# Performance work log

Hardware: AMD Instinct MI355X
Metric: run time of the kernel (lower is better)

Reference implementation:

```python
import jax, jax.numpy as jnp
import numpy as np

B, T, H, P, N = 32, 512, 128, 16, 16
D = 4 * H


def _lstm(x, Wih, Whh, bih, bhh):
    # standard torch-style LSTM, batch_first input x: [B, T, 1], zero init state
    Bz = x.shape[0]
    Hh = Whh.shape[1]
    h0 = jnp.zeros((Bz, Hh), x.dtype)

    def step(carry, xt):
        h, c = carry
        g = xt @ Wih.T + bih + h @ Whh.T + bhh  # [B, 4H], gate order i,f,g,o
        i, f, gg, o = jnp.split(g, 4, axis=-1)
        c = jax.nn.sigmoid(f) * c + jax.nn.sigmoid(i) * jnp.tanh(gg)
        h = jax.nn.sigmoid(o) * jnp.tanh(c)
        return (h, c), h

    _, hs = jax.lax.scan(step, (h0, h0), jnp.swapaxes(x, 0, 1))
    return jnp.swapaxes(hs, 0, 1)  # [B, T, H]


def _forward(Y, Xp, Xn, Xi, init_c, init_h, Wih, Whh, bih, bhh,
             Wc, Uc, bc, Wg, Ug, bg, Wf, Uf, bf, Wo, Uo, bo, Wa,
             Watt, batt, vatt, W1, b1, W2, b2, W3, b3):
    run = lambda x: _lstm(x, Wih, Whh, bih, bhh)
    Y1 = run(Y)                                              # [B,T,H]
    Xi1 = run(Xi)
    Xp1 = jnp.mean(jax.vmap(run)(jnp.moveaxis(Xp, 1, 0)), axis=0)  # mean over P stocks
    Xn1 = jnp.mean(jax.vmap(run)(jnp.moveaxis(Xn, 1, 0)), axis=0)
    result = jnp.concatenate([Y1, Xp1, Xn1, Xi1], axis=2)    # [B,T,4H]

    Hh = Wa.shape[0]

    def mi_step(carry, xt):  # Mi-LSTM cell: 4 input streams with gated-candidate attention
        c, h = carry
        xs = xt.reshape(xt.shape[0], 4, Hh)                  # split 4H into 4 streams
        cand = jnp.tanh(jnp.einsum('bkh,khj->bkj', xs, Wc) + jnp.einsum('bh,khj->bkj', h, Uc) + bc)
        ig = jax.nn.sigmoid(jnp.einsum('bkh,khj->bkj', xs, Wg) + jnp.einsum('bh,khj->bkj', h, Ug) + bg)
        l = ig * cand                                        # [B,4,H]
        a = jax.nn.softmax(jnp.einsum('bkj,bj->bk', l, c @ Wa), axis=1)
        lmix = jnp.einsum('bk,bkj->bj', a, l)
        f = jax.nn.sigmoid(xt @ Wf + h @ Uf + bf)
        o = jax.nn.sigmoid(xt @ Wo + h @ Uo + bo)
        c = f * c + lmix
        h = o * jnp.tanh(c)
        return (c, h), h

    _, hs = jax.lax.scan(mi_step, (init_c, init_h), jnp.swapaxes(result, 0, 1))
    Y2 = jnp.swapaxes(hs, 0, 1)                              # [B,T,H]

    # temporal attention over the Mi-LSTM outputs
    scores = jnp.tanh(Y2 @ Watt + batt) @ vatt               # [B,T]
    attw = jax.nn.softmax(scores, axis=1)
    Y3 = jnp.einsum('bt,bth->bh', attw, Y2)                  # [B,H]

    hm = jax.nn.relu(Y3 @ W1 + b1)
    hm = jax.nn.relu(hm @ W2 + b2)
    return hm @ W3 + b3                                      # [B,1]


def setup_inputs() -> dict:
    key = jax.random.key(0)
    ks = jax.random.split(key, 24)
    u = lambda k, s: jax.random.uniform(k, s, dtype=jnp.float32)
    nr = lambda k, s: jax.random.normal(k, s, dtype=jnp.float32) * 0.05
    z = lambda s: jnp.zeros(s, jnp.float32)
    return {
        'Y': u(ks[0], (B, T, 1)), 'Xp': u(ks[1], (B, P, T, 1)), 'Xn': u(ks[2], (B, N, T, 1)),
        'Xi': u(ks[3], (B, T, 1)), 'Target': u(ks[4], (B, 1)),
        'init_c': u(ks[5], (B, H)), 'init_h': u(ks[6], (B, H)),
        'Wih': nr(ks[7], (4 * H, 1)), 'Whh': nr(ks[8], (4 * H, H)), 'bih': z(4 * H), 'bhh': z(4 * H),
        'Wc': nr(ks[9], (4, H, H)), 'Uc': nr(ks[10], (4, H, H)), 'bc': z((4, H)),
        'Wg': nr(ks[11], (4, H, H)), 'Ug': nr(ks[12], (4, H, H)), 'bg': z((4, H)),
        'Wf': nr(ks[13], (D, H)), 'Uf': nr(ks[14], (H, H)), 'bf': z(H),
        'Wo': nr(ks[15], (D, H)), 'Uo': nr(ks[16], (H, H)), 'bo': z(H),
        'Wa': nr(ks[17], (H, H)),
        'Watt': nr(ks[18], (H, H)), 'batt': z(H), 'vatt': nr(ks[19], (H,)),
        'W1': nr(ks[20], (H, H)), 'b1': z(H),
        'W2': nr(ks[21], (H, H)), 'b2': z(H),
        'W3': nr(ks[22], (H, 1)), 'b3': z(1),
    }


def reference(Y, Xp, Xn, Xi, Target, init_c, init_h, Wih, Whh, bih, bhh,
              Wc, Uc, bc, Wg, Ug, bg, Wf, Uf, bf, Wo, Uo, bo, Wa,
              Watt, batt, vatt, W1, b1, W2, b2, W3, b3):
    out = _forward(Y, Xp, Xn, Xi, init_c, init_h, Wih, Whh, bih, bhh,
                   Wc, Uc, bc, Wg, Ug, bg, Wf, Uf, bf, Wo, Uo, bo, Wa,
                   Watt, batt, vatt, W1, b1, W2, b2, W3, b3)
    loss = jnp.mean((out - Target) ** 2)
    return out, loss
```

## Files before the change

kernel.cpp:

```cpp
#include <hip/hip_runtime.h>
#include <hip/hip_fp16.h>

typedef _Float16 half8 __attribute__((ext_vector_type(8)));
typedef float float4_ __attribute__((ext_vector_type(4)));

__device__ __forceinline__ float rcp_(float x) { return __builtin_amdgcn_rcpf(x); }
__device__ __forceinline__ float sigf(float x) { return rcp_(1.f + __expf(-x)); }
__device__ __forceinline__ float tanhf2(float x) {
  x = fminf(fmaxf(x, -15.f), 15.f);
  float e = __expf(-2.f * x);
  return (1.f - e) * rcp_(1.f + e);
}

#define DOT2F16(acc, w, h) asm("v_dot2_f32_f16 %0, %1, %2, %0" : "+v"(acc) : "v"(w), "v"(h))

__global__ __launch_bounds__(512, 2)
void k1_lstm(const float* __restrict__ Y, const float* __restrict__ Xp,
             const float* __restrict__ Xn, const float* __restrict__ Xi,
             const float* __restrict__ Wih, const float* __restrict__ Whh,
             const float* __restrict__ bih, const float* __restrict__ bhh,
             _Float16* __restrict__ result)
{
  __shared__ float x_lds[16][513];
  __shared__ _Float16 hbuf[2][16][136];

  const int tid  = threadIdx.x;
  const int wv   = tid >> 6;
  const int lane = tid & 63;
  const int cl   = lane & 15;
  const int rowg = lane >> 4;
  const int bid  = blockIdx.x;

  const float* xsrc; int slot; int do_mean; int b_out_base;
  if (bid < 2)       { xsrc = Y  + (size_t)(bid * 16) * 512;        slot = 0; do_mean = 0; b_out_base = bid * 16; }
  else if (bid < 4)  { xsrc = Xi + (size_t)((bid - 2) * 16) * 512;  slot = 3; do_mean = 0; b_out_base = (bid - 2) * 16; }
  else if (bid < 36) { xsrc = Xp + (size_t)((bid - 4) * 16) * 512;  slot = 1; do_mean = 1; b_out_base = bid - 4; }
  else               { xsrc = Xn + (size_t)((bid - 36) * 16) * 512; slot = 2; do_mean = 1; b_out_base = bid - 36; }

  for (int i = tid; i < 16 * 512; i += 512) {
    int r = i >> 9, t = i & 511;
    x_lds[r][t] = xsrc[r * 512 + t];
  }
  for (int i = tid; i < 16 * 136; i += 512) {
    hbuf[0][i / 136][i % 136] = (_Float16)0.f;
  }

  const int cg = wv * 16 + cl;
  half8 bw[4][4];
  #pragma unroll
  for (int g = 0; g < 4; ++g) {
    #pragma unroll
    for (int kc = 0; kc < 4; ++kc) {
      const float* p = Whh + (size_t)(g * 128 + cg) * 128 + kc * 32 + rowg * 8;
      half8 v;
      #pragma unroll
      for (int j = 0; j < 8; ++j) v[j] = (_Float16)p[j];
      bw[g][kc] = v;
    }
  }
  float wih_r[4], bias_r[4];
  #pragma unroll
  for (int g = 0; g < 4; ++g) {
    wih_r[g]  = Wih[g * 128 + cg];
    bias_r[g] = bih[g * 128 + cg] + bhh[g * 128 + cg];
  }

  float c_reg[4] = {0.f, 0.f, 0.f, 0.f};
  float hvp[4] = {0.f, 0.f, 0.f, 0.f};
  float sprev = 0.f;
  __syncthreads();

  for (int t = 0; t < 512; ++t) {
    if (t > 0) {
      if (!do_mean) {
        #pragma unroll
        for (int i = 0; i < 4; ++i) {
          int b = b_out_base + rowg * 4 + i;
          result[(((size_t)b * 512 + (t - 1)) * 4 + slot) * 128 + cg] = (_Float16)hvp[i];
        }
      } else {
        if (rowg == 0)
          result[(((size_t)b_out_base * 512 + (t - 1)) * 4 + slot) * 128 + cg] = (_Float16)sprev;
      }
    }

    const int cur = t & 1;
    half8 a[4];
    #pragma unroll
    for (int kc = 0; kc < 4; ++kc)
      a[kc] = *(const half8*)&hbuf[cur][cl][kc * 32 + rowg * 8];

    float4_ acc[4];
    #pragma unroll
    for (int g = 0; g < 4; ++g) {
      float4_ z = {0.f, 0.f, 0.f, 0.f};
      #pragma unroll
      for (int kc = 0; kc < 4; ++kc)
        z = __builtin_amdgcn_mfma_f32_16x16x32_f16(a[kc], bw[g][kc], z, 0, 0, 0);
      acc[g] = z;
    }

    float hv[4];
    #pragma unroll
    for (int i = 0; i < 4; ++i) {
      const int row = rowg * 4 + i;
      float x  = x_lds[row][t];
      float ui = acc[0][i] + x * wih_r[0] + bias_r[0];
      float uf = acc[1][i] + x * wih_r[1] + bias_r[1];
      float ug = acc[2][i] + x * wih_r[2] + bias_r[2];
      float uo = acc[3][i] + x * wih_r[3] + bias_r[3];
      float ii = sigf(ui), ff = sigf(uf), gg = tanhf2(ug), oo = sigf(uo);
      float c  = ff * c_reg[i] + ii * gg;
      c_reg[i] = c;
      float h  = oo * tanhf2(c);
      hv[i] = h;
      hbuf[cur ^ 1][row][cg] = (_Float16)h;
    }

    if (!do_mean) {
      #pragma unroll
      for (int i = 0; i < 4; ++i) hvp[i] = hv[i];
    } else {
      float s = hv[0] + hv[1] + hv[2] + hv[3];
      s += __shfl_xor(s, 16, 64);
      s += __shfl_xor(s, 32, 64);
      sprev = s * 0.0625f;
    }
    __syncthreads();
  }

  if (!do_mean) {
    #pragma unroll
    for (int i = 0; i < 4; ++i) {
      int b = b_out_base + rowg * 4 + i;
      result[(((size_t)b * 512 + 511) * 4 + slot) * 128 + cg] = (_Float16)hvp[i];
    }
  } else {
    if (rowg == 0)
      result[(((size_t)b_out_base * 512 + 511) * 4 + slot) * 128 + cg] = (_Float16)sprev;
  }
}

__global__ __launch_bounds__(512, 2)
void k2_gemm(const _Float16* __restrict__ result,
             const float* __restrict__ Wc, const float* __restrict__ Wg,
             const float* __restrict__ Wf, const float* __restrict__ Wo,
             _Float16* __restrict__ candX, _Float16* __restrict__ igX,
             _Float16* __restrict__ fX, _Float16* __restrict__ oX)
{
  __shared__ _Float16 a_lds[128][136];
  __shared__ _Float16 bt_lds[256][136];

  const int tid   = threadIdx.x;
  const int lane  = tid & 63;
  const int wv    = tid >> 6;
  const int cl    = lane & 15, rowg = lane >> 4;
  const int mtile = blockIdx.x;
  const int role  = blockIdx.y;

  const int nchunks = (role == 0) ? 4 : 1;
  const int kstream = role - 1;

  float4_ acc[16];
  #pragma unroll
  for (int n = 0; n < 16; ++n) acc[n] = (float4_){0.f, 0.f, 0.f, 0.f};

  for (int ch = 0; ch < nchunks; ++ch) {
    const int koff = (role == 0) ? ch * 128 : kstream * 128;
    for (int i = tid; i < 1024; i += 512) {
      int r = i >> 3, v8 = i & 7;
      half8 val = *(const half8*)&result[((size_t)(mtile * 128 + r)) * 512 + koff + v8 * 8];
      *(half8*)&a_lds[r][v8 * 8] = val;
    }
    for (int i = tid; i < 128 * 256; i += 512) {
      int n = i & 255, kk = i >> 8;
      float w;
      if (role == 0) {
        w = (n < 128) ? Wf[(size_t)(ch * 128 + kk) * 128 + n]
                      : Wo[(size_t)(ch * 128 + kk) * 128 + (n - 128)];
      } else {
        w = (n < 128) ? Wc[(size_t)(kstream * 128 + kk) * 128 + n]
                      : Wg[(size_t)(kstream * 128 + kk) * 128 + (n - 128)];
      }
      bt_lds[n][kk] = (_Float16)w;
    }
    __syncthreads();
    #pragma unroll
    for (int kc = 0; kc < 4; ++kc) {
      half8 a = *(const half8*)&a_lds[wv * 16 + cl][kc * 32 + rowg * 8];
      #pragma unroll
      for (int n = 0; n < 16; ++n) {
        half8 bb = *(const half8*)&bt_lds[n * 16 + cl][kc * 32 + rowg * 8];
        acc[n] = __builtin_amdgcn_mfma_f32_16x16x32_f16(a, bb, acc[n], 0, 0, 0);
      }
    }
    __syncthreads();
  }

  #pragma unroll
  for (int n = 0; n < 16; ++n) {
    int col = n * 16 + cl;
    #pragma unroll
    for (int i = 0; i < 4; ++i) {
      size_t r = (size_t)mtile * 128 + wv * 16 + rowg * 4 + i;
      _Float16 v = (_Float16)acc[n][i];
      if (role == 0) {
        if (col < 128) fX[r * 128 + col] = v;
        else           oX[r * 128 + (col - 128)] = v;
      } else {
        if (col < 128) candX[(r * 4 + kstream) * 128 + col] = v;
        else           igX  [(r * 4 + kstream) * 128 + (col - 128)] = v;
      }
    }
  }
}

#define PRELOAD(arr, sbase)                                                 \
  {                                                                         \
    const int s = tid + sbase;                                              \
    const float* src; float mul = 1.f;                                      \
    if (s < 512)       src = Uc + (s >> 7) * 16384 + (s & 127);             \
    else if (s < 1024) src = Ug + ((s >> 7) - 4) * 16384 + (s & 127);       \
    else if (s < 1152) src = Uf + (s - 1024);                               \
    else if (s < 1280) src = Uo + (s - 1152);                               \
    else if (s < 1408) src = Wa + (s - 1280);                               \
    else             { src = Wa; mul = 0.f; }                               \
    _Pragma("unroll")                                                       \
    for (int d = 0; d < 64; ++d) {                                          \
      union { _Float16 h[2]; unsigned u; } cv;                              \
      cv.h[0] = (_Float16)(src[(2 * d) * 128] * mul);                       \
      cv.h[1] = (_Float16)(src[(2 * d + 1) * 128] * mul);                   \
      arr[d] = cv.u;                                                        \
    }                                                                       \
  }

__global__ __launch_bounds__(512, 1)
void k3_scan(const float* __restrict__ Uc, const float* __restrict__ Ug,
             const float* __restrict__ Uf, const float* __restrict__ Uo,
             const float* __restrict__ Wa,
             const float* __restrict__ bc, const float* __restrict__ bg,
             const float* __restrict__ bfv, const float* __restrict__ bov,
             const float* __restrict__ init_c, const float* __restrict__ init_h,
             const _Float16* __restrict__ candX, const _Float16* __restrict__ igX,
             const _Float16* __restrict__ fX, const _Float16* __restrict__ oX,
             _Float16* __restrict__ Y2)
{
  __shared__ __align__(16) unsigned h_pk[64];
  __shared__ __align__(16) unsigned c_pk[64];
  __shared__ float c_f32[128];
  __shared__ float raw[1536];
  __shared__ float part2[2][4];

  const int tid = threadIdx.x;
  const int b   = blockIdx.x;

  unsigned wpk0[64], wpk1[64], wpk2[64];
  PRELOAD(wpk0, 0)
  PRELOAD(wpk1, 512)
  PRELOAD(wpk2, 1024)

  float bc_r[4] = {0, 0, 0, 0}, bg_r[4] = {0, 0, 0, 0}, bf_r = 0.f, bo_r = 0.f;
  if (tid < 128) {
    #pragma unroll
    for (int k = 0; k < 4; ++k) { bc_r[k] = bc[k * 128 + tid]; bg_r[k] = bg[k * 128 + tid]; }
    bf_r = bfv[tid]; bo_r = bov[tid];
    c_f32[tid] = init_c[b * 128 + tid];
  }
  if (tid < 64) {
    union { _Float16 h[2]; unsigned u; } hp, cp;
    hp.h[0] = (_Float16)init_h[b * 128 + 2 * tid];
    hp.h[1] = (_Float16)init_h[b * 128 + 2 * tid + 1];
    cp.h[0] = (_Float16)init_c[b * 128 + 2 * tid];
    cp.h[1] = (_Float16)init_c[b * 128 + 2 * tid + 1];
    h_pk[tid] = hp.u;
    c_pk[tid] = cp.u;
  }
  __syncthreads();

  const int slot3 = tid + 1024;
  float hprev = 0.f;

  for (int t = 0; t < 512; ++t) {
    if (t > 0 && tid < 128)
      Y2[((size_t)b * 512 + (t - 1)) * 128 + tid] = (_Float16)hprev;

    float cx[4] = {0, 0, 0, 0}, gx[4] = {0, 0, 0, 0}, fx = 0.f, ox = 0.f;
    if (tid < 128) {
      size_t r = (size_t)b * 512 + t;
      #pragma unroll
      for (int k = 0; k < 4; ++k) {
        cx[k] = (float)candX[(r * 4 + k) * 128 + tid];
        gx[k] = (float)igX  [(r * 4 + k) * 128 + tid];
      }
      fx = (float)fX[r * 128 + tid];
      ox = (float)oX[r * 128 + tid];
    }

    float a1 = 0.f, a2 = 0.f, a3 = 0.f;
    {
      const uint4* hp4 = (const uint4*)h_pk;
      if (tid < 256 || tid >= 384) {
        #pragma unroll
        for (int g = 0; g < 16; ++g) {
          uint4 hv = hp4[g];
          DOT2F16(a1, wpk0[4*g+0], hv.x); DOT2F16(a2, wpk1[4*g+0], hv.x); DOT2F16(a3, wpk2[4*g+0], hv.x);
          DOT2F16(a1, wpk0[4*g+1], hv.y); DOT2F16(a2, wpk1[4*g+1], hv.y); DOT2F16(a3, wpk2[4*g+1], hv.y);
          DOT2F16(a1, wpk0[4*g+2], hv.z); DOT2F16(a2, wpk1[4*g+2], hv.z); DOT2F16(a3, wpk2[4*g+2], hv.z);
          DOT2F16(a1, wpk0[4*g+3], hv.w); DOT2F16(a2, wpk1[4*g+3], hv.w); DOT2F16(a3, wpk2[4*g+3], hv.w);
        }
      } else {
        const uint4* cp4 = (const uint4*)c_pk;
        #pragma unroll
        for (int g = 0; g < 16; ++g) {
          uint4 hv = hp4[g]; uint4 hc = cp4[g];
          DOT2F16(a1, wpk0[4*g+0], hv.x); DOT2F16(a2, wpk1[4*g+0], hv.x); DOT2F16(a3, wpk2[4*g+0], hc.x);
          DOT2F16(a1, wpk0[4*g+1], hv.y); DOT2F16(a2, wpk1[4*g+1], hv.y); DOT2F16(a3, wpk2[4*g+1], hc.y);
          DOT2F16(a1, wpk0[4*g+2], hv.z); DOT2F16(a2, wpk1[4*g+2], hv.z); DOT2F16(a3, wpk2[4*g+2], hc.z);
          DOT2F16(a1, wpk0[4*g+3], hv.w); DOT2F16(a2, wpk1[4*g+3], hv.w); DOT2F16(a3, wpk2[4*g+3], hc.w);
        }
      }
    }
    raw[tid]       = a1;
    raw[tid + 512] = a2;
    raw[slot3]     = a3;
    __syncthreads();

    float l0 = 0.f, l1 = 0.f, l2 = 0.f, l3 = 0.f, fj = 0.f, oj = 0.f;
    if (tid < 128) {
      float cand[4], ig[4];
      #pragma unroll
      for (int k = 0; k < 4; ++k) {
        float uc = cx[k] + raw[k * 128 + tid] + bc_r[k];
        float ui = gx[k] + raw[512 + k * 128 + tid] + bg_r[k];
        cand[k] = tanhf2(uc);
        ig[k]   = sigf(ui);
      }
      l0 = ig[0] * cand[0]; l1 = ig[1] * cand[1];
      l2 = ig[2] * cand[2]; l3 = ig[3] * cand[3];
      float cwa = raw[1280 + tid];
      float p0 = l0 * cwa, p1 = l1 * cwa, p2 = l2 * cwa, p3 = l3 * cwa;
      #pragma unroll
      for (int m = 1; m < 64; m <<= 1) {
        p0 += __shfl_xor(p0, m, 64);
        p1 += __shfl_xor(p1, m, 64);
        p2 += __shfl_xor(p2, m, 64);
        p3 += __shfl_xor(p3, m, 64);
      }
      if ((tid & 63) == 0) {
        part2[tid >> 6][0] = p0; part2[tid >> 6][1] = p1;
        part2[tid >> 6][2] = p2; part2[tid >> 6][3] = p3;
      }
      fj = sigf(fx + raw[1024 + tid] + bf_r);
      oj = sigf(ox + raw[1152 + tid] + bo_r);
    }
    __syncthreads();

    if (tid < 128) {
      float d0 = part2[0][0] + part2[1][0];
      float d1 = part2[0][1] + part2[1][1];
      float d2 = part2[0][2] + part2[1][2];
      float d3 = part2[0][3] + part2[1][3];
      float mx = fmaxf(fmaxf(d0, d1), fmaxf(d2, d3));
      float e0 = __expf(d0 - mx), e1 = __expf(d1 - mx);
      float e2 = __expf(d2 - mx), e3 = __expf(d3 - mx);
      float inv = rcp_(e0 + e1 + e2 + e3);
      float lmix = (e0 * l0 + e1 * l1 + e2 * l2 + e3 * l3) * inv;
      float c = fj * c_f32[tid] + lmix;
      c_f32[tid] = c;
      float h = oj * tanhf2(c);
      ((_Float16*)h_pk)[tid] = (_Float16)h;
      ((_Float16*)c_pk)[tid] = (_Float16)c;
      hprev = h;
    }
    __syncthreads();
  }

  if (tid < 128)
    Y2[((size_t)b * 512 + 511) * 128 + tid] = (_Float16)hprev;
}

__global__ __launch_bounds__(256, 1)
void k4_attn(const _Float16* __restrict__ Y2,
             const float* __restrict__ Watt, const float* __restrict__ batt,
             const float* __restrict__ vatt,
             const float* __restrict__ W1, const float* __restrict__ b1,
             const float* __restrict__ W2, const float* __restrict__ b2,
             const float* __restrict__ W3, const float* __restrict__ b3,
             float* __restrict__ out)
{
  __shared__ _Float16 wt_lds[128][136];
  __shared__ float sc[512];
  __shared__ float red[8];
  __shared__ float y3[128];
  __shared__ float hm[128];

  const int tid = threadIdx.x;
  const int b   = blockIdx.x;
  const int lane = tid & 63, wv = tid >> 6;
  const int cl = lane & 15, rowg = lane >> 4;

  for (int i = tid; i < 128 * 128; i += 256) {
    int h = i >> 7, j = i & 127;
    wt_lds[j][h] = (_Float16)Watt[h * 128 + j];
  }
  __syncthreads();

  half8 bw[8][4];
  #pragma unroll
  for (int n = 0; n < 8; ++n)
    #pragma unroll
    for (int kc = 0; kc < 4; ++kc)
      bw[n][kc] = *(const half8*)&wt_lds[n * 16 + cl][kc * 32 + rowg * 8];
  float battr[8], vattr[8];
  #pragma unroll
  for (int n = 0; n < 8; ++n) { battr[n] = batt[n * 16 + cl]; vattr[n] = vatt[n * 16 + cl]; }

  for (int mt = wv * 8; mt < wv * 8 + 8; ++mt) {
    half8 a[4];
    #pragma unroll
    for (int kc = 0; kc < 4; ++kc)
      a[kc] = *(const half8*)&Y2[((size_t)b * 512 + mt * 16 + cl) * 128 + kc * 32 + rowg * 8];
    float sp[4] = {0.f, 0.f, 0.f, 0.f};
    #pragma unroll
    for (int n = 0; n < 8; ++n) {
      float4_ acc = {0.f, 0.f, 0.f, 0.f};
      #pragma unroll
      for (int kc = 0; kc < 4; ++kc)
        acc = __builtin_amdgcn_mfma_f32_16x16x32_f16(a[kc], bw[n][kc], acc, 0, 0, 0);
      #pragma unroll
      for (int i = 0; i < 4; ++i)
        sp[i] += tanhf2(acc[i] + battr[n]) * vattr[n];
    }
    #pragma unroll
    for (int i = 0; i < 4; ++i) {
      #pragma unroll
      for (int m = 1; m < 16; m <<= 1) sp[i] += __shfl_xor(sp[i], m, 64);
    }
    if (cl == 0) {
      #pragma unroll
      for (int i = 0; i < 4; ++i) sc[mt * 16 + rowg * 4 + i] = sp[i];
    }
  }
  __syncthreads();

  float v0 = sc[tid], v1 = sc[tid + 256];
  float mx = fmaxf(v0, v1);
  #pragma unroll
  for (int m = 1; m < 64; m <<= 1) mx = fmaxf(mx, __shfl_xor(mx, m, 64));
  if (lane == 0) red[wv] = mx;
  __syncthreads();
  mx = fmaxf(fmaxf(red[0], red[1]), fmaxf(red[2], red[3]));
  float e0 = __expf(v0 - mx), e1 = __expf(v1 - mx);
  float s = e0 + e1;
  #pragma unroll
  for (int m = 1; m < 64; m <<= 1) s += __shfl_xor(s, m, 64);
  __syncthreads();
  if (lane == 0) red[wv] = s;
  __syncthreads();
  float inv = rcp_(red[0] + red[1] + red[2] + red[3]);
  sc[tid] = e0 * inv;
  sc[tid + 256] = e1 * inv;
  __syncthreads();

  {
    int h = tid & 127, part = tid >> 7;
    float acc = 0.f;
    for (int t = part * 256; t < part * 256 + 256; ++t)
      acc += sc[t] * (float)Y2[((size_t)b * 512 + t) * 128 + h];
    if (part == 0) y3[h] = acc;
    __syncthreads();
    if (part == 1) y3[h] += acc;
    __syncthreads();
  }

  if (tid < 128) {
    float a1 = 0.f;
    for (int h2 = 0; h2 < 128; ++h2) a1 += y3[h2] * W1[h2 * 128 + tid];
    hm[tid] = fmaxf(a1 + b1[tid], 0.f);
  }
  __syncthreads();
  if (tid < 128) {
    float a2 = 0.f;
    for (int h2 = 0; h2 < 128; ++h2) a2 += hm[h2] * W2[h2 * 128 + tid];
    a2 = fmaxf(a2 + b2[tid], 0.f);
    float p = a2 * W3[tid];
    #pragma unroll
    for (int m = 1; m < 64; m <<= 1) p += __shfl_xor(p, m, 64);
    if ((tid & 63) == 0) red[4 + (tid >> 6)] = p;
  }
  __syncthreads();
  if (tid == 0) out[b] = red[4] + red[5] + b3[0];
}

__global__ void k5_loss(const float* __restrict__ out, const float* __restrict__ target,
                        float* __restrict__ loss_out)
{
  int l = threadIdx.x;
  float v = 0.f;
  if (l < 32) { float d = out[l] - target[l]; v = d * d; }
  #pragma unroll
  for (int m = 1; m < 64; m <<= 1) v += __shfl_xor(v, m, 64);
  if (l == 0) loss_out[0] = v * (1.f / 32.f);
}

extern "C" void kernel_launch(void* const* d_in, const int* in_sizes, int n_in,
                              void* d_out, int out_size, void* d_ws, size_t ws_size,
                              hipStream_t stream)
{
  const float* Y      = (const float*)d_in[0];
  const float* Xp     = (const float*)d_in[1];
  const float* Xn     = (const float*)d_in[2];
  const float* Xi     = (const float*)d_in[3];
  const float* Target = (const float*)d_in[4];
  const float* init_c = (const float*)d_in[5];
  const float* init_h = (const float*)d_in[6];
  const float* Wih    = (const float*)d_in[7];
  const float* Whh    = (const float*)d_in[8];
  const float* bih    = (const float*)d_in[9];
  const float* bhh    = (const float*)d_in[10];
  const float* Wc     = (const float*)d_in[11];
  const float* Uc     = (const float*)d_in[12];
  const float* bc     = (const float*)d_in[13];
  const float* Wg     = (const float*)d_in[14];
  const float* Ug     = (const float*)d_in[15];
  const float* bg     = (const float*)d_in[16];
  const float* Wf     = (const float*)d_in[17];
  const float* Uf     = (const float*)d_in[18];
  const float* bf     = (const float*)d_in[19];
  const float* Wo     = (const float*)d_in[20];
  const float* Uo     = (const float*)d_in[21];
  const float* bo     = (const float*)d_in[22];
  const float* Wa     = (const float*)d_in[23];
  const float* Watt   = (const float*)d_in[24];
  const float* batt   = (const float*)d_in[25];
  const float* vatt   = (const float*)d_in[26];
  const float* W1     = (const float*)d_in[27];
  const float* b1     = (const float*)d_in[28];
  const float* W2     = (const float*)d_in[29];
  const float* b2     = (const float*)d_in[30];
  const float* W3     = (const float*)d_in[31];
  const float* b3     = (const float*)d_in[32];

  char* ws = (char*)d_ws;
  _Float16* result = (_Float16*)(ws);
  _Float16* candX  = (_Float16*)(ws + ((size_t)16 << 20));
  _Float16* igX    = (_Float16*)(ws + ((size_t)32 << 20));
  _Float16* fXp    = (_Float16*)(ws + ((size_t)48 << 20));
  _Float16* oXp    = (_Float16*)(ws + ((size_t)52 << 20));
  _Float16* Y2     = (_Float16*)(ws + ((size_t)56 << 20));
  float* outp = (float*)d_out;

  k1_lstm<<<dim3(68), dim3(512), 0, stream>>>(Y, Xp, Xn, Xi, Wih, Whh, bih, bhh, result);
  k2_gemm<<<dim3(128, 5), dim3(512), 0, stream>>>(result, Wc, Wg, Wf, Wo, candX, igX, fXp, oXp);
  k3_scan<<<dim3(32), dim3(512), 0, stream>>>(Uc, Ug, Uf, Uo, Wa, bc, bg, bf, bo,
                                              init_c, init_h, candX, igX, fXp, oXp, Y2);
  k4_attn<<<dim3(32), dim3(256), 0, stream>>>(Y2, Watt, batt, vatt, W1, b1, W2, b2, W3, b3, outp);
  k5_loss<<<dim3(1), dim3(64), 0, stream>>>(outp, Target, outp + 32);
}
```

Before: 1.711 ms.

## Compute Mi-LSTM recurrent matvec with MFMA instead of per-thread dot2

In the recurrent scan, the per-thread v_dot2 matrix-vector products against the packed Uc/Ug/Uf/Uo/Wa weights are replaced with 16x16x32 f16 MFMA instructions. Weights are preloaded as register-resident A fragments, 11 column groups per wave. The h and c vectors are broadcast as the B operand, and only column 0 of each result is written to LDS. The aim is to move the serial per-step matvec onto matrix cores and cut VALU issue and LDS broadcast reads. The cost is that 15/16 of each MFMA's output columns are redundant, and every step still runs chained MFMA latency.

```diff
diff --git a/kernel.cpp b/kernel.cpp
--- a/kernel.cpp
+++ b/kernel.cpp
@@ -11,8 +11,6 @@
   float e = __expf(-2.f * x);
   return (1.f - e) * rcp_(1.f + e);
 }
-
-#define DOT2F16(acc, w, h) asm("v_dot2_f32_f16 %0, %1, %2, %0" : "+v"(acc) : "v"(w), "v"(h))
 
 __global__ __launch_bounds__(512, 2)
 void k1_lstm(const float* __restrict__ Y, const float* __restrict__ Xp,
@@ -214,25 +212,6 @@
     }
   }
 }
-
-#define PRELOAD(arr, sbase)                                                 \
-  {                                                                         \
-    const int s = tid + sbase;                                              \
-    const float* src; float mul = 1.f;                                      \
-    if (s < 512)       src = Uc + (s >> 7) * 16384 + (s & 127);             \
-    else if (s < 1024) src = Ug + ((s >> 7) - 4) * 16384 + (s & 127);       \
-    else if (s < 1152) src = Uf + (s - 1024);                               \
-    else if (s < 1280) src = Uo + (s - 1152);                               \
-    else if (s < 1408) src = Wa + (s - 1280);                               \
-    else             { src = Wa; mul = 0.f; }                               \
-    _Pragma("unroll")                                                       \
-    for (int d = 0; d < 64; ++d) {                                          \
-      union { _Float16 h[2]; unsigned u; } cv;                              \
-      cv.h[0] = (_Float16)(src[(2 * d) * 128] * mul);                       \
-      cv.h[1] = (_Float16)(src[(2 * d + 1) * 128] * mul);                   \
-      arr[d] = cv.u;                                                        \
-    }                                                                       \
-  }
 
 __global__ __launch_bounds__(512, 1)
 void k3_scan(const float* __restrict__ Uc, const float* __restrict__ Ug,
@@ -248,16 +227,35 @@
   __shared__ __align__(16) unsigned h_pk[64];
   __shared__ __align__(16) unsigned c_pk[64];
   __shared__ float c_f32[128];
-  __shared__ float raw[1536];
+  __shared__ __align__(16) float raw[1408];
   __shared__ float part2[2][4];
 
-  const int tid = threadIdx.x;
-  const int b   = blockIdx.x;
-
-  unsigned wpk0[64], wpk1[64], wpk2[64];
-  PRELOAD(wpk0, 0)
-  PRELOAD(wpk1, 512)
-  PRELOAD(wpk2, 1024)
+  const int tid  = threadIdx.x;
+  const int b    = blockIdx.x;
+  const int wv   = tid >> 6;
+  const int lane = tid & 63;
+  const int cl   = lane & 15;
+  const int rowg = lane >> 4;
+
+  half8 wfrag[11][4];
+  #pragma unroll
+  for (int gi = 0; gi < 11; ++gi) {
+    const int col = (wv * 11 + gi) * 16 + cl;
+    const float* src;
+    if (col < 512)       src = Uc + (col >> 7) * 16384 + (col & 127);
+    else if (col < 1024) src = Ug + ((col >> 7) - 4) * 16384 + (col & 127);
+    else if (col < 1152) src = Uf + (col - 1024);
+    else if (col < 1280) src = Uo + (col - 1152);
+    else                 src = Wa + (col - 1280);
+    #pragma unroll
+    for (int kc = 0; kc < 4; ++kc) {
+      half8 v;
+      #pragma unroll
+      for (int j = 0; j < 8; ++j)
+        v[j] = (_Float16)src[(kc * 32 + rowg * 8 + j) * 128];
+      wfrag[gi][kc] = v;
+    }
+  }
 
   float bc_r[4] = {0, 0, 0, 0}, bg_r[4] = {0, 0, 0, 0}, bf_r = 0.f, bo_r = 0.f;
   if (tid < 128) {
@@ -277,7 +275,6 @@
   }
   __syncthreads();
 
-  const int slot3 = tid + 1024;
   float hprev = 0.f;
 
   for (int t = 0; t < 512; ++t) {
@@ -296,33 +293,32 @@
       ox = (float)oX[r * 128 + tid];
     }
 
-    float a1 = 0.f, a2 = 0.f, a3 = 0.f;
     {
       const uint4* hp4 = (const uint4*)h_pk;
-      if (tid < 256 || tid >= 384) {
-        #pragma unroll
-        for (int g = 0; g < 16; ++g) {
-          uint4 hv = hp4[g];
-          DOT2F16(a1, wpk0[4*g+0], hv.x); DOT2F16(a2, wpk1[4*g+0], hv.x); DOT2F16(a3, wpk2[4*g+0], hv.x);
-          DOT2F16(a1, wpk0[4*g+1], hv.y); DOT2F16(a2, wpk1[4*g+1], hv.y); DOT2F16(a3, wpk2[4*g+1], hv.y);
-          DOT2F16(a1, wpk0[4*g+2], hv.z); DOT2F16(a2, wpk1[4*g+2], hv.z); DOT2F16(a3, wpk2[4*g+2], hv.z);
-          DOT2F16(a1, wpk0[4*g+3], hv.w); DOT2F16(a2, wpk1[4*g+3], hv.w); DOT2F16(a3, wpk2[4*g+3], hv.w);
+      const uint4* cp4 = (const uint4*)c_pk;
+      union { uint4 u; half8 h; } hb[4], cb[4];
+      #pragma unroll
+      for (int kc = 0; kc < 4; ++kc) {
+        hb[kc].u = hp4[kc * 4 + rowg];
+        cb[kc].u = cp4[kc * 4 + rowg];
+      }
+      #pragma unroll
+      for (int gi = 0; gi < 11; ++gi) {
+        const int g = wv * 11 + gi;
+        float4_ acc = {0.f, 0.f, 0.f, 0.f};
+        if (g < 80) {
+          #pragma unroll
+          for (int kc = 0; kc < 4; ++kc)
+            acc = __builtin_amdgcn_mfma_f32_16x16x32_f16(wfrag[gi][kc], hb[kc].h, acc, 0, 0, 0);
+        } else {
+          #pragma unroll
+          for (int kc = 0; kc < 4; ++kc)
+            acc = __builtin_amdgcn_mfma_f32_16x16x32_f16(wfrag[gi][kc], cb[kc].h, acc, 0, 0, 0);
         }
-      } else {
-        const uint4* cp4 = (const uint4*)c_pk;
-        #pragma unroll
-        for (int g = 0; g < 16; ++g) {
-          uint4 hv = hp4[g]; uint4 hc = cp4[g];
-          DOT2F16(a1, wpk0[4*g+0], hv.x); DOT2F16(a2, wpk1[4*g+0], hv.x); DOT2F16(a3, wpk2[4*g+0], hc.x);
-          DOT2F16(a1, wpk0[4*g+1], hv.y); DOT2F16(a2, wpk1[4*g+1], hv.y); DOT2F16(a3, wpk2[4*g+1], hc.y);
-          DOT2F16(a1, wpk0[4*g+2], hv.z); DOT2F16(a2, wpk1[4*g+2], hv.z); DOT2F16(a3, wpk2[4*g+2], hc.z);
-          DOT2F16(a1, wpk0[4*g+3], hv.w); DOT2F16(a2, wpk1[4*g+3], hv.w); DOT2F16(a3, wpk2[4*g+3], hc.w);
-        }
-      }
-    }
-    raw[tid]       = a1;
-    raw[tid + 512] = a2;
-    raw[slot3]     = a3;
+        if (cl == 0)
+          *(float4_*)&raw[g * 16 + rowg * 4] = acc;
+      }
+    }
     __syncthreads();
 
     float l0 = 0.f, l1 = 0.f, l2 = 0.f, l3 = 0.f, fj = 0.f, oj = 0.f;
```

After: 1.850 ms. 1.08x slower.
